# Kernel optimization log

Measured on AMD Instinct MI355X. Metric: run time of the kernel, lower is better.

The kernel has to match this reference:

```python
import jax, jax.numpy as jnp
import numpy as np

EMBED_DIM = 1024
B, T = 8, 2048


def setup_inputs() -> dict:
    key = jax.random.key(0)
    kx, kw, kb = jax.random.split(key, 3)
    x = jax.random.normal(kx, (B, T, EMBED_DIM), dtype=jnp.float32)
    # nn.Linear(embed_dim, 3*embed_dim): weight [3E, E], bias [3E]
    bound = 1.0 / np.sqrt(EMBED_DIM)
    W = jax.random.uniform(kw, (3 * EMBED_DIM, EMBED_DIM), minval=-bound, maxval=bound, dtype=jnp.float32)
    b = jax.random.uniform(kb, (3 * EMBED_DIM,), minval=-bound, maxval=bound, dtype=jnp.float32)
    return {"x": x, "W": W, "b": b}


def reference(x, W, b):
    E = x.shape[-1]
    qkv = jnp.einsum('bte,fe->btf', x, W) + b            # [B,T,3E]
    q, k, v = jnp.split(qkv, 3, axis=-1)                 # each [B,T,E]
    scale = 1.0 / jnp.sqrt(jnp.asarray(E, dtype=x.dtype))
    scores = jnp.einsum('bqe,bke->bqk', q, k) * scale    # [B,T,T]
    Tq = x.shape[1]
    causal = jnp.tril(jnp.ones((Tq, Tq), dtype=bool))
    scores = jnp.where(causal[None, :, :], scores, jnp.asarray(-jnp.inf, dtype=x.dtype))
    attn = jax.nn.softmax(scores, axis=-1)
    y = jnp.einsum('bqk,bke->bqe', attn, v)              # [B,T,E]
    return y
```

## Files before the change

kernel.cpp:

```cpp
#include <hip/hip_runtime.h>

typedef unsigned short u16;
typedef unsigned int u32;
typedef __attribute__((ext_vector_type(4))) float f32x4;
typedef __attribute__((ext_vector_type(8))) short bf16x8;

#define T_DIM 2048
#define E_DIM 1024
#define NBATCH 8
#define BK 32
#define BUF 32768
#define CORE_LDS (3 * BUF)

struct alignas(8)  U16x4 { u16 x, y, z, w; };
struct alignas(16) F32x4 { float x, y, z, w; };

__device__ __forceinline__ u16 f2bf(float f) {
  u32 u = __float_as_uint(f);
  u += 0x7FFFu + ((u >> 16) & 1u);
  return (u16)(u >> 16);
}

__device__ __forceinline__ void gld16(u16* lds, const u16* g) {
  __builtin_amdgcn_global_load_lds((const __attribute__((address_space(1))) void*)g,
                                   (__attribute__((address_space(3))) void*)lds, 16, 0, 0);
}

__device__ __forceinline__ u32 swz7(u32 x) { return x ^ (((x >> 7) & 7u) << 4); }

__device__ __forceinline__ int xcd_swz(int orig, int nwg) {
  int q = nwg >> 3, r = nwg & 7;
  int x = orig & 7, l = orig >> 3;
  return (x < r ? x * (q + 1) : r * (q + 1) + (x - r) * q) + l;
}

#define LGKM0_PIN() do { asm volatile("s_waitcnt lgkmcnt(0)" ::: "memory"); \
                         __builtin_amdgcn_sched_barrier(0); } while (0)

template <typename HOOK>
__device__ __forceinline__ void gemm256(const u16* __restrict__ A, const u16* __restrict__ B,
                                        int lda, int ldb, int nK, char* lds0, f32x4 acc[8][4],
                                        HOOK&& hook)
{
  const int tid = threadIdx.x, lane = tid & 63, wave = tid >> 6;
  const int wr = wave >> 2, wc = wave & 3;

  const u16* sAp[2]; const u16* sBp[2];
#pragma unroll
  for (int c = 0; c < 2; ++c) {
    u32 L = (u32)(c * 8192 + tid * 16);
    u32 g = swz7(L);
    sAp[c] = A + (size_t)(g >> 6) * lda + ((g & 63u) >> 1);
    sBp[c] = B + (size_t)(g >> 6) * ldb + ((g & 63u) >> 1);
  }
  const u32 doff = (u32)tid * 16u;

  auto stageA = [&](char* buf, int t) {
#pragma unroll
    for (int c = 0; c < 2; ++c)
      gld16((u16*)(buf + c * 8192 + doff), sAp[c] + t * BK);
  };
  auto stageB = [&](char* buf, int t) {
#pragma unroll
    for (int c = 0; c < 2; ++c)
      gld16((u16*)(buf + 16384 + c * 8192 + doff), sBp[c] + t * BK);
  };

  const u32 cb = (u32)(lane >> 4) * 16u;
  u32 aoff[8], boff[4];
#pragma unroll
  for (int m = 0; m < 8; ++m)
    aoff[m] = swz7((u32)(wr * 128 + m * 16 + (lane & 15)) * 64u + cb);
#pragma unroll
  for (int n = 0; n < 4; ++n)
    boff[n] = 16384u + swz7((u32)(wc * 64 + n * 16 + (lane & 15)) * 64u + cb);

  stageA(lds0, 0); stageB(lds0, 0);
  stageA(lds0 + BUF, 1); stageB(lds0 + BUF, 1);

  int bc = 0;
  bf16x8 a[4], b[4];
  for (int t = 0; t < nK; ++t) {
    char* bufR = lds0 + bc * BUF;
    int b2 = bc + 2; if (b2 >= 3) b2 -= 3;
    char* bufW = lds0 + b2 * BUF;

    if (t + 1 < nK) asm volatile("s_waitcnt vmcnt(4)" ::: "memory");
    else            asm volatile("s_waitcnt vmcnt(0)" ::: "memory");
    __builtin_amdgcn_s_barrier();
    __builtin_amdgcn_sched_barrier(0);

    hook(t);

    if (t + 2 < nK) stageA(bufW, t + 2);
#pragma unroll
    for (int j = 0; j < 4; ++j) a[j] = *(const bf16x8*)(bufR + aoff[j]);
#pragma unroll
    for (int n = 0; n < 4; ++n) b[n] = *(const bf16x8*)(bufR + boff[n]);
    LGKM0_PIN();
    __builtin_amdgcn_s_setprio(1);
#pragma unroll
    for (int j = 0; j < 4; ++j)
#pragma unroll
      for (int n = 0; n < 4; ++n)
        acc[j][n] = __builtin_amdgcn_mfma_f32_16x16x32_bf16(a[j], b[n], acc[j][n], 0, 0, 0);
    __builtin_amdgcn_s_setprio(0);
    __builtin_amdgcn_sched_barrier(0);

    if (t + 2 < nK) stageB(bufW, t + 2);
#pragma unroll
    for (int j = 0; j < 4; ++j) a[j] = *(const bf16x8*)(bufR + aoff[4 + j]);
    LGKM0_PIN();
    __builtin_amdgcn_s_setprio(1);
#pragma unroll
    for (int j = 0; j < 4; ++j)
#pragma unroll
      for (int n = 0; n < 4; ++n)
        acc[4 + j][n] = __builtin_amdgcn_mfma_f32_16x16x32_bf16(a[j], b[n], acc[4 + j][n], 0, 0, 0);
    __builtin_amdgcn_s_setprio(0);
    __builtin_amdgcn_sched_barrier(0);

    bc = bc + 1 == 3 ? 0 : bc + 1;
  }
}

struct NoHook { __device__ void operator()(int) const {} };

__global__ __launch_bounds__(256) void k_cvt(const float* __restrict__ in, u16* __restrict__ out, int n4)
{
  int i = blockIdx.x * 256 + threadIdx.x;
  if (i >= n4) return;
  F32x4 v = *(const F32x4*)&in[(size_t)i * 4];
  U16x4 o;
  o.x = f2bf(v.x); o.y = f2bf(v.y); o.z = f2bf(v.z); o.w = f2bf(v.w);
  *(U16x4*)&out[(size_t)i * 4] = o;
}

__global__ __launch_bounds__(512, 2) void k_qkv(const u16* __restrict__ Xb, const u16* __restrict__ Wb,
                                                const float* __restrict__ bias,
                                                u16* __restrict__ Q, u16* __restrict__ Kmat,
                                                u16* __restrict__ Vt)
{
  __shared__ __align__(16) char lds[CORE_LDS];
  const int wg = xcd_swz(blockIdx.x, gridDim.x);
  const int my = wg / 12, nx = wg % 12;
  const int m0 = my * 256, n0 = nx * 256;
  const int tid = threadIdx.x, lane = tid & 63, wave = tid >> 6;
  const int wr = wave >> 2, wc = wave & 3;
  f32x4 acc[8][4] = {};
  gemm256(Xb + (size_t)m0 * E_DIM, Wb + (size_t)n0 * E_DIM, E_DIM, E_DIM, E_DIM / BK,
          lds, acc, NoHook{});
  __syncthreads();

  char* wsl = lds + wave * 8192;
  const int region = nx >> 2;
  const int nlb = (n0 & (E_DIM - 1)) + wc * 64;

  if (region < 2) {
    u16* dst = region ? Kmat : Q;
#pragma unroll
    for (int p = 0; p < 2; ++p) {
#pragma unroll
      for (int n = 0; n < 4; ++n) {
        const float bn = bias[n0 + wc * 64 + n * 16 + (lane & 15)];
#pragma unroll
        for (int mm = 0; mm < 4; ++mm)
#pragma unroll
          for (int r = 0; r < 4; ++r) {
            const int rl = mm * 16 + ((lane >> 4) << 2) + r;
            const int cl = n * 16 + (lane & 15);
            u32 byte = (u32)(rl * 128 + cl * 2) ^ (u32)((rl & 7) << 4);
            *(u16*)(wsl + byte) = f2bf(acc[p * 4 + mm][n][r] + bn);
          }
      }
      asm volatile("s_waitcnt lgkmcnt(0)" ::: "memory");
      const int rowb = m0 + wr * 128 + p * 64;
#pragma unroll
      for (int it = 0; it < 8; ++it) {
        const int rl = it * 8 + (lane >> 3);
        const int c16 = lane & 7;
        u32 byte = (u32)(rl * 128 + c16 * 16) ^ (u32)((rl & 7) << 4);
        bf16x8 v = *(const bf16x8*)(wsl + byte);
        *(bf16x8*)&dst[(size_t)(rowb + rl) * E_DIM + nlb + c16 * 8] = v;
      }
      if (p == 0) asm volatile("s_waitcnt lgkmcnt(0)" ::: "memory");
    }
  } else {
    const int bl = m0 >> 11;
    const int tb = (m0 & (T_DIM - 1)) + wr * 128;
#pragma unroll
    for (int p = 0; p < 2; ++p) {
#pragma unroll
      for (int n = 0; n < 4; ++n) {
        const float bn = bias[n0 + wc * 64 + n * 16 + (lane & 15)];
        const int e_l = n * 16 + (lane & 15);
#pragma unroll
        for (int mm = 0; mm < 4; ++mm)
#pragma unroll
          for (int r = 0; r < 4; ++r) {
            const int tl = mm * 16 + ((lane >> 4) << 2) + r;
            u32 byte = (u32)(e_l * 128 + tl * 2) ^ (u32)((e_l & 7) << 4);
            *(u16*)(wsl + byte) = f2bf(acc[p * 4 + mm][n][r] + bn);
          }
      }
      asm volatile("s_waitcnt lgkmcnt(0)" ::: "memory");
#pragma unroll
      for (int it = 0; it < 8; ++it) {
        const int e_l = it * 8 + (lane >> 3);
        const int t16 = lane & 7;
        u32 byte = (u32)(e_l * 128 + t16 * 16) ^ (u32)((e_l & 7) << 4);
        bf16x8 v = *(const bf16x8*)(wsl + byte);
        *(bf16x8*)&Vt[((size_t)bl * E_DIM + nlb + e_l) * T_DIM + tb + p * 64 + t16 * 8] = v;
      }
      if (p == 0) asm volatile("s_waitcnt lgkmcnt(0)" ::: "memory");
    }
  }
}

__global__ __launch_bounds__(512, 2) void k_sp(const u16* __restrict__ Q, const u16* __restrict__ Kmat,
                                               u16* __restrict__ P, float* __restrict__ mc,
                                               float* __restrict__ lc)
{
  __shared__ __align__(16) char lds[CORE_LDS];
  const int wg = xcd_swz(blockIdx.x, gridDim.x);
  const int b = wg / 36;
  const int ti = wg % 36;
  int iq = 0;
  while ((iq + 1) * (iq + 2) / 2 <= ti) ++iq;
  const int ik = ti - iq * (iq + 1) / 2;
  const int tid = threadIdx.x, lane = tid & 63, wave = tid >> 6;
  const int wr = wave >> 2, wc = wave & 3;
  f32x4 acc[8][4] = {};
  const u16* Qp = Q    + (size_t)b * T_DIM * E_DIM + (size_t)iq * 256 * E_DIM;
  const u16* Kp = Kmat + (size_t)b * T_DIM * E_DIM + (size_t)ik * 256 * E_DIM;
  gemm256(Qp, Kp, E_DIM, E_DIM, E_DIM / BK, lds, acc, NoHook{});
  __syncthreads();

  const float scale = 0.03125f;
#pragma unroll
  for (int m = 0; m < 8; ++m)
#pragma unroll
    for (int n = 0; n < 4; ++n)
#pragma unroll
      for (int r = 0; r < 4; ++r) acc[m][n][r] *= scale;
  if (ik == iq) {
#pragma unroll
    for (int n = 0; n < 4; ++n) {
      const int kg = wc * 64 + n * 16 + (lane & 15);
#pragma unroll
      for (int m = 0; m < 8; ++m) {
        const int qg0 = wr * 128 + m * 16 + ((lane >> 4) << 2);
#pragma unroll
        for (int r = 0; r < 4; ++r)
          if (kg > qg0 + r) acc[m][n][r] = -3.4e38f;
      }
    }
  }

  float* red  = (float*)lds;
  float* red2 = (float*)lds + 1024;
  float M[8][4];
#pragma unroll
  for (int m = 0; m < 8; ++m)
#pragma unroll
    for (int r = 0; r < 4; ++r) {
      float v = fmaxf(fmaxf(acc[m][0][r], acc[m][1][r]), fmaxf(acc[m][2][r], acc[m][3][r]));
#pragma unroll
      for (int off = 1; off <= 8; off <<= 1) v = fmaxf(v, __shfl_xor(v, off, 64));
      M[m][r] = v;
    }
  if ((lane & 15) == 0) {
#pragma unroll
    for (int m = 0; m < 8; ++m)
#pragma unroll
      for (int r = 0; r < 4; ++r)
        red[wc * 256 + wr * 128 + m * 16 + ((lane >> 4) << 2) + r] = M[m][r];
  }
  __syncthreads();
#pragma unroll
  for (int m = 0; m < 8; ++m)
#pragma unroll
    for (int r = 0; r < 4; ++r) {
      const int row = wr * 128 + m * 16 + ((lane >> 4) << 2) + r;
      M[m][r] = fmaxf(fmaxf(red[row], red[256 + row]), fmaxf(red[512 + row], red[768 + row]));
    }

  float Ls[8][4];
#pragma unroll
  for (int m = 0; m < 8; ++m)
#pragma unroll
    for (int r = 0; r < 4; ++r) {
      float s = 0.f;
#pragma unroll
      for (int n = 0; n < 4; ++n) {
        float e = __expf(acc[m][n][r] - M[m][r]);
        acc[m][n][r] = e;
        s += e;
      }
#pragma unroll
      for (int off = 1; off <= 8; off <<= 1) s += __shfl_xor(s, off, 64);
      Ls[m][r] = s;
    }
  if ((lane & 15) == 0) {
#pragma unroll
    for (int m = 0; m < 8; ++m)
#pragma unroll
      for (int r = 0; r < 4; ++r)
        red2[wc * 256 + wr * 128 + m * 16 + ((lane >> 4) << 2) + r] = Ls[m][r];
  }
  __syncthreads();
  if (wc == 0 && (lane & 15) == 0) {
#pragma unroll
    for (int m = 0; m < 8; ++m)
#pragma unroll
      for (int r = 0; r < 4; ++r) {
        const int row = wr * 128 + m * 16 + ((lane >> 4) << 2) + r;
        const float l = red2[row] + red2[256 + row] + red2[512 + row] + red2[768 + row];
        const size_t idx = ((size_t)b * T_DIM + iq * 256 + row) * 8 + ik;
        mc[idx] = M[m][r];
        lc[idx] = l;
      }
  }
  __syncthreads();

  u16* Pb = P + (size_t)b * T_DIM * T_DIM;
  char* wsl = lds + 16384 + wave * 8192;
#pragma unroll
  for (int p = 0; p < 2; ++p) {
#pragma unroll
    for (int n = 0; n < 4; ++n)
#pragma unroll
      for (int mm = 0; mm < 4; ++mm)
#pragma unroll
        for (int r = 0; r < 4; ++r) {
          const int rl = mm * 16 + ((lane >> 4) << 2) + r;
          const int cl = n * 16 + (lane & 15);
          u32 byte = (u32)(rl * 128 + cl * 2) ^ (u32)((rl & 7) << 4);
          *(u16*)(wsl + byte) = f2bf(acc[p * 4 + mm][n][r]);
        }
    asm volatile("s_waitcnt lgkmcnt(0)" ::: "memory");
    const int rowb = iq * 256 + wr * 128 + p * 64;
    const int colb = ik * 256 + wc * 64;
#pragma unroll
    for (int it = 0; it < 8; ++it) {
      const int rl = it * 8 + (lane >> 3);
      const int c16 = lane & 7;
      u32 byte = (u32)(rl * 128 + c16 * 16) ^ (u32)((rl & 7) << 4);
      bf16x8 v = *(const bf16x8*)(wsl + byte);
      *(bf16x8*)&Pb[(size_t)(rowb + rl) * T_DIM + colb + c16 * 8] = v;
    }
    if (p == 0) asm volatile("s_waitcnt lgkmcnt(0)" ::: "memory");
  }
}

__global__ __launch_bounds__(256) void k_finish(const float* __restrict__ mc, const float* __restrict__ lc,
                                                float* __restrict__ fin)
{
  const int rg = blockIdx.x * 256 + threadIdx.x;
  const int q = rg & (T_DIM - 1);
  const int C = (q >> 8) + 1;
  const float* m = mc + (size_t)rg * 8;
  const float* l = lc + (size_t)rg * 8;
  float M = -3.4e38f;
  for (int c = 0; c < C; ++c) M = fmaxf(M, m[c]);
  float L = 0.f;
  for (int c = 0; c < C; ++c) L += l[c] * __expf(m[c] - M);
  fin[rg] = __expf(m[C - 1] - M) / L;
}

__global__ __launch_bounds__(512, 2) void k_pv(const u16* __restrict__ P, const u16* __restrict__ Vt,
                                               const float* __restrict__ mc, const float* __restrict__ fin,
                                               float* __restrict__ out, int batch0)
{
  __shared__ __align__(16) char lds[CORE_LDS + 8192];
  const int wg = xcd_swz(blockIdx.x, gridDim.x);
  const int bl = wg >> 5, rr = wg & 31;
  const int iq = rr >> 2, ie = rr & 3;
  const int tid = threadIdx.x, lane = tid & 63, wave = tid >> 6;
  const int wr = wave >> 2, wc = wave & 3;

  float* ldsM = (float*)(lds + CORE_LDS);
  const float* mrow = mc + ((size_t)bl * T_DIM + iq * 256) * 8;
  for (int i = tid; i < 2048; i += 512) ldsM[i] = mrow[i];
  asm volatile("s_waitcnt vmcnt(0) lgkmcnt(0)" ::: "memory");
  __builtin_amdgcn_s_barrier();

  f32x4 acc[8][4] = {};
  const u16* Ap = P  + (size_t)bl * T_DIM * T_DIM + (size_t)iq * 256 * T_DIM;
  const u16* Bp = Vt + (size_t)bl * E_DIM * T_DIM + (size_t)ie * 256 * T_DIM;

  auto rescale = [&](int t) {
    if (t > 0 && (t & 7) == 0) {
      const int c = t >> 3;
#pragma unroll
      for (int m = 0; m < 8; ++m)
#pragma unroll
        for (int r = 0; r < 4; ++r) {
          const int row = wr * 128 + m * 16 + ((lane >> 4) << 2) + r;
          const float h = __expf(ldsM[row * 8 + (c - 1)] - ldsM[row * 8 + c]);
#pragma unroll
          for (int n = 0; n < 4; ++n) acc[m][n][r] *= h;
        }
    }
  };
  gemm256(Ap, Bp, T_DIM, T_DIM, (iq + 1) * 8, lds, acc, rescale);

#pragma unroll
  for (int m = 0; m < 8; ++m) {
    const int qg0 = iq * 256 + wr * 128 + m * 16 + ((lane >> 4) << 2);
#pragma unroll
    for (int r = 0; r < 4; ++r) {
      const int qg = qg0 + r;
      const float il = fin[bl * T_DIM + qg];
      float* orow = out + ((size_t)(batch0 + bl) * T_DIM + qg) * E_DIM;
#pragma unroll
      for (int n = 0; n < 4; ++n) {
        const int eg = ie * 256 + wc * 64 + n * 16 + (lane & 15);
        orow[eg] = acc[m][n][r] * il;
      }
    }
  }
}

extern "C" void kernel_launch(void* const* d_in, const int* in_sizes, int n_in,
                              void* d_out, int out_size, void* d_ws, size_t ws_size,
                              hipStream_t stream)
{
  const float* x    = (const float*)d_in[0];
  const float* W    = (const float*)d_in[1];
  const float* bias = (const float*)d_in[2];
  float* out = (float*)d_out;

  char* ws = (char*)d_ws;
  const size_t ALIGN = 256;
  auto up = [&](size_t v) { return (v + ALIGN - 1) & ~(ALIGN - 1); };

  const size_t szWb = up((size_t)3 * E_DIM * E_DIM * 2);
  const size_t szX  = up((size_t)T_DIM * E_DIM * 2);
  const size_t szP  = up((size_t)T_DIM * T_DIM * 2);
  const size_t szM  = up((size_t)T_DIM * 8 * 4);
  const size_t szI  = up((size_t)T_DIM * 4);
  const size_t perB = 4 * szX + szP + 2 * szM + szI;

  int nb = 1;
  for (int cand = NBATCH; cand >= 1; --cand) {
    if (szWb + (size_t)cand * perB <= ws_size) { nb = cand; break; }
  }

  u16* Wb = (u16*)ws;
  {
    int n4 = 3 * E_DIM * E_DIM / 4;
    k_cvt<<<(n4 + 255) / 256, 256, 0, stream>>>(W, Wb, n4);
  }

  for (int b0 = 0; b0 < NBATCH; b0 += nb) {
    const int nbc = (NBATCH - b0 < nb) ? (NBATCH - b0) : nb;
    size_t o = szWb;
    u16* Xb    = (u16*)(ws + o);   o += (size_t)nbc * szX;
    u16* Qb    = (u16*)(ws + o);   o += (size_t)nbc * szX;
    u16* Kb    = (u16*)(ws + o);   o += (size_t)nbc * szX;
    u16* Vt    = (u16*)(ws + o);   o += (size_t)nbc * szX;
    u16* P     = (u16*)(ws + o);   o += (size_t)nbc * szP;
    float* mcA = (float*)(ws + o); o += (size_t)nbc * szM;
    float* lcA = (float*)(ws + o); o += (size_t)nbc * szM;
    float* fin = (float*)(ws + o); o += (size_t)nbc * szI;

    {
      int n4 = nbc * T_DIM * E_DIM / 4;
      k_cvt<<<(n4 + 255) / 256, 256, 0, stream>>>(x + (size_t)b0 * T_DIM * E_DIM, Xb, n4);
    }
    k_qkv<<<dim3(96 * nbc), 512, 0, stream>>>(Xb, Wb, bias, Qb, Kb, Vt);
    k_sp<<<dim3(36 * nbc), 512, 0, stream>>>(Qb, Kb, P, mcA, lcA);
    k_finish<<<dim3(nbc * T_DIM / 256), 256, 0, stream>>>(mcA, lcA, fin);
    k_pv<<<dim3(32 * nbc), 512, 0, stream>>>(P, Vt, mcA, fin, out, b0);
  }
}
```

Before: 270.2 us.

## Balance causal PV work with paired 128-row tiles and regroup QKV tile mapping

```diff
diff --git a/kernel.cpp b/kernel.cpp
--- a/kernel.cpp
+++ b/kernel.cpp
@@ -11,6 +11,8 @@
 #define BK 32
 #define BUF 32768
 #define CORE_LDS (3 * BUF)
+#define BUFP 24576
+#define COREP_LDS (3 * BUFP)
 
 struct alignas(8)  U16x4 { u16 x, y, z, w; };
 struct alignas(16) F32x4 { float x, y, z, w; };
@@ -124,6 +126,93 @@
   }
 }
 
+template <typename HOOK>
+__device__ __forceinline__ void gemm128n(const u16* __restrict__ A, const u16* __restrict__ B,
+                                         int lda, int ldb, int nK, char* lds0, f32x4 acc[4][4],
+                                         HOOK&& hook)
+{
+  const int tid = threadIdx.x, lane = tid & 63, wave = tid >> 6;
+  const int wr = wave >> 2, wc = wave & 3;
+
+  const u16* sA0; const u16* sBp[2];
+  {
+    u32 g = swz7((u32)tid * 16u);
+    sA0 = A + (size_t)(g >> 6) * lda + ((g & 63u) >> 1);
+  }
+#pragma unroll
+  for (int c = 0; c < 2; ++c) {
+    u32 g = swz7((u32)(c * 8192 + tid * 16));
+    sBp[c] = B + (size_t)(g >> 6) * ldb + ((g & 63u) >> 1);
+  }
+  const u32 doff = (u32)tid * 16u;
+
+  auto stageA = [&](char* buf, int t) {
+    gld16((u16*)(buf + doff), sA0 + t * BK);
+  };
+  auto stageB = [&](char* buf, int t) {
+#pragma unroll
+    for (int c = 0; c < 2; ++c)
+      gld16((u16*)(buf + 8192 + c * 8192 + doff), sBp[c] + t * BK);
+  };
+
+  const u32 cb = (u32)(lane >> 4) * 16u;
+  u32 aoff[4], boff[4];
+#pragma unroll
+  for (int m = 0; m < 4; ++m)
+    aoff[m] = swz7((u32)(wr * 64 + m * 16 + (lane & 15)) * 64u + cb);
+#pragma unroll
+  for (int n = 0; n < 4; ++n)
+    boff[n] = 8192u + swz7((u32)(wc * 64 + n * 16 + (lane & 15)) * 64u + cb);
+
+  stageA(lds0, 0); stageB(lds0, 0);
+  stageA(lds0 + BUFP, 1); stageB(lds0 + BUFP, 1);
+
+  int bc = 0;
+  bf16x8 a[2], b[4];
+  for (int t = 0; t < nK; ++t) {
+    char* bufR = lds0 + bc * BUFP;
+    int b2 = bc + 2; if (b2 >= 3) b2 -= 3;
+    char* bufW = lds0 + b2 * BUFP;
+
+    if (t + 1 < nK) asm volatile("s_waitcnt vmcnt(3)" ::: "memory");
+    else            asm volatile("s_waitcnt vmcnt(0)" ::: "memory");
+    __builtin_amdgcn_s_barrier();
+    __builtin_amdgcn_sched_barrier(0);
+
+    hook(t);
+
+    if (t + 2 < nK) stageA(bufW, t + 2);
+    a[0] = *(const bf16x8*)(bufR + aoff[0]);
+    a[1] = *(const bf16x8*)(bufR + aoff[1]);
+#pragma unroll
+    for (int n = 0; n < 4; ++n) b[n] = *(const bf16x8*)(bufR + boff[n]);
+    LGKM0_PIN();
+    __builtin_amdgcn_s_setprio(1);
+#pragma unroll
+    for (int j = 0; j < 2; ++j)
+#pragma unroll
+      for (int n = 0; n < 4; ++n)
+        acc[j][n] = __builtin_amdgcn_mfma_f32_16x16x32_bf16(a[j], b[n], acc[j][n], 0, 0, 0);
+    __builtin_amdgcn_s_setprio(0);
+    __builtin_amdgcn_sched_barrier(0);
+
+    if (t + 2 < nK) stageB(bufW, t + 2);
+    a[0] = *(const bf16x8*)(bufR + aoff[2]);
+    a[1] = *(const bf16x8*)(bufR + aoff[3]);
+    LGKM0_PIN();
+    __builtin_amdgcn_s_setprio(1);
+#pragma unroll
+    for (int j = 0; j < 2; ++j)
+#pragma unroll
+      for (int n = 0; n < 4; ++n)
+        acc[2 + j][n] = __builtin_amdgcn_mfma_f32_16x16x32_bf16(a[j], b[n], acc[2 + j][n], 0, 0, 0);
+    __builtin_amdgcn_s_setprio(0);
+    __builtin_amdgcn_sched_barrier(0);
+
+    bc = bc + 1 == 3 ? 0 : bc + 1;
+  }
+}
+
 struct NoHook { __device__ void operator()(int) const {} };
 
 __global__ __launch_bounds__(256) void k_cvt(const float* __restrict__ in, u16* __restrict__ out, int n4)
@@ -142,8 +231,17 @@
                                                 u16* __restrict__ Vt)
 {
   __shared__ __align__(16) char lds[CORE_LDS];
-  const int wg = xcd_swz(blockIdx.x, gridDim.x);
-  const int my = wg / 12, nx = wg % 12;
+  int my, nx;
+  if (gridDim.x == 768) {
+    const int x = blockIdx.x & 7, tau = blockIdx.x >> 3;
+    const int st = tau >> 4, w = tau & 15;
+    const int gm = st / 3, gn = st % 3;
+    my = x * 8 + gm * 4 + (w >> 2);
+    nx = gn * 4 + (w & 3);
+  } else {
+    const int wg = xcd_swz(blockIdx.x, gridDim.x);
+    my = wg / 12; nx = wg % 12;
+  }
   const int m0 = my * 256, n0 = nx * 256;
   const int tid = threadIdx.x, lane = tid & 63, wave = tid >> 6;
   const int wr = wave >> 2, wc = wave & 3;
@@ -372,51 +470,59 @@
                                                const float* __restrict__ mc, const float* __restrict__ fin,
                                                float* __restrict__ out, int batch0)
 {
-  __shared__ __align__(16) char lds[CORE_LDS + 8192];
+  __shared__ __align__(16) char lds[COREP_LDS + 4096];
   const int wg = xcd_swz(blockIdx.x, gridDim.x);
   const int bl = wg >> 5, rr = wg & 31;
-  const int iq = rr >> 2, ie = rr & 3;
+  const int pr = rr >> 2, ie = rr & 3;
   const int tid = threadIdx.x, lane = tid & 63, wave = tid >> 6;
   const int wr = wave >> 2, wc = wave & 3;
 
-  float* ldsM = (float*)(lds + CORE_LDS);
-  const float* mrow = mc + ((size_t)bl * T_DIM + iq * 256) * 8;
-  for (int i = tid; i < 2048; i += 512) ldsM[i] = mrow[i];
-  asm volatile("s_waitcnt vmcnt(0) lgkmcnt(0)" ::: "memory");
-  __builtin_amdgcn_s_barrier();
-
-  f32x4 acc[8][4] = {};
-  const u16* Ap = P  + (size_t)bl * T_DIM * T_DIM + (size_t)iq * 256 * T_DIM;
+  float* ldsM = (float*)(lds + COREP_LDS);
   const u16* Bp = Vt + (size_t)bl * E_DIM * T_DIM + (size_t)ie * 256 * T_DIM;
 
-  auto rescale = [&](int t) {
-    if (t > 0 && (t & 7) == 0) {
-      const int c = t >> 3;
-#pragma unroll
-      for (int m = 0; m < 8; ++m)
-#pragma unroll
-        for (int r = 0; r < 4; ++r) {
-          const int row = wr * 128 + m * 16 + ((lane >> 4) << 2) + r;
-          const float h = __expf(ldsM[row * 8 + (c - 1)] - ldsM[row * 8 + c]);
-#pragma unroll
-          for (int n = 0; n < 4; ++n) acc[m][n][r] *= h;
+#pragma unroll
+  for (int mem = 0; mem < 2; ++mem) {
+    const int iq = mem ? 15 - pr : pr;
+    const int nch = (iq >> 1) + 1;
+
+    __syncthreads();
+    const float* mrow = mc + ((size_t)bl * T_DIM + iq * 128) * 8;
+    for (int i = tid; i < 1024; i += 512) ldsM[i] = mrow[i];
+    asm volatile("s_waitcnt vmcnt(0) lgkmcnt(0)" ::: "memory");
+    __builtin_amdgcn_s_barrier();
+
+    f32x4 acc[4][4] = {};
+    const u16* Ap = P + (size_t)bl * T_DIM * T_DIM + (size_t)iq * 128 * T_DIM;
+
+    auto rescale = [&](int t) {
+      if (t > 0 && (t & 7) == 0) {
+        const int c = t >> 3;
+#pragma unroll
+        for (int m = 0; m < 4; ++m)
+#pragma unroll
+          for (int r = 0; r < 4; ++r) {
+            const int row = wr * 64 + m * 16 + ((lane >> 4) << 2) + r;
+            const float h = __expf(ldsM[row * 8 + (c - 1)] - ldsM[row * 8 + c]);
+#pragma unroll
+            for (int n = 0; n < 4; ++n) acc[m][n][r] *= h;
+          }
+      }
+    };
+    gemm128n(Ap, Bp, T_DIM, T_DIM, nch * 8, lds, acc, rescale);
+
+#pragma unroll
+    for (int m = 0; m < 4; ++m) {
+      const int qg0 = iq * 128 + wr * 64 + m * 16 + ((lane >> 4) << 2);
+#pragma unroll
+      for (int r = 0; r < 4; ++r) {
+        const int qg = qg0 + r;
+        const float il = fin[bl * T_DIM + qg];
+        float* orow = out + ((size_t)(batch0 + bl) * T_DIM + qg) * E_DIM;
+#pragma unroll
+        for (int n = 0; n < 4; ++n) {
+          const int eg = ie * 256 + wc * 64 + n * 16 + (lane & 15);
+          orow[eg] = acc[m][n][r] * il;
         }
-    }
-  };
-  gemm256(Ap, Bp, T_DIM, T_DIM, (iq + 1) * 8, lds, acc, rescale);
-
-#pragma unroll
-  for (int m = 0; m < 8; ++m) {
-    const int qg0 = iq * 256 + wr * 128 + m * 16 + ((lane >> 4) << 2);
-#pragma unroll
-    for (int r = 0; r < 4; ++r) {
-      const int qg = qg0 + r;
-      const float il = fin[bl * T_DIM + qg];
-      float* orow = out + ((size_t)(batch0 + bl) * T_DIM + qg) * E_DIM;
-#pragma unroll
-      for (int n = 0; n < 4; ++n) {
-        const int eg = ie * 256 + wc * 64 + n * 16 + (lane & 15);
-        orow[eg] = acc[m][n][r] * il;
       }
     }
   }
```

After: 258.6 us. 4.3% less time.
